# Kernel optimization log

Hardware: AMD Instinct MI355X
Metric: run time of the kernel (lower is better)

## Reference

```python
import jax, jax.numpy as jnp
import numpy as np
import itertools


def setup_inputs() -> dict:
    key = jax.random.key(0)
    k1, k2 = jax.random.split(key)
    vol = jax.random.normal(k1, (2, 160, 192, 224, 2), dtype=jnp.float32)
    trf = jax.random.normal(k2, (2, 160, 192, 224, 3), dtype=jnp.float32)
    return {"vol": vol, "trf": trf}


def _interpn_linear(vol, loc):
    """N-D multilinear interpolation of vol [*shape, C] at float locations.

    loc: list of ndims arrays, each [*shape], giving absolute sample coords.
    Out-of-domain points are clamped to the boundary (fill_value=None).
    Matches neurite's interpn('linear') math.
    """
    shape = vol.shape[:-1]
    ndims = len(shape)
    C = vol.shape[-1]
    maxs = [s - 1 for s in shape]

    # clip sample locations into the valid domain
    loc = [jnp.clip(l, 0.0, float(m)) for l, m in zip(loc, maxs)]
    loc0 = [jnp.clip(jnp.floor(l), 0.0, float(m)) for l, m in zip(loc, maxs)]
    loc1 = [jnp.clip(l0 + 1.0, 0.0, float(m)) for l0, m in zip(loc0, maxs)]
    # corner-0 weight is (loc1 - loc), corner-1 weight is its complement
    w_c0 = [l1 - l for l1, l in zip(loc1, loc)]
    w_c1 = [1.0 - w for w in w_c0]

    idx0 = [l.astype(jnp.int32) for l in loc0]
    idx1 = [l.astype(jnp.int32) for l in loc1]

    # row-major strides for flat gather
    strides = np.concatenate([np.cumprod(np.array(shape[::-1]))[::-1][1:], [1]]).astype(np.int32)
    vol_flat = vol.reshape(-1, C)

    out = jnp.zeros(shape + (C,), dtype=vol.dtype)
    for corner in itertools.product((0, 1), repeat=ndims):
        flat_idx = 0
        wt = 1.0
        for d in range(ndims):
            i = idx0[d] if corner[d] == 0 else idx1[d]
            w = w_c0[d] if corner[d] == 0 else w_c1[d]
            flat_idx = flat_idx + i * int(strides[d])
            wt = wt * w
        gathered = jnp.take(vol_flat, flat_idx, axis=0)  # [*shape, C]
        out = out + wt[..., None] * gathered
    return out


def reference(vol, trf):
    # single_transform=True: only the first batch element is used
    v = vol[0]   # [D1, D2, D3, C]
    t = trf[0]   # [D1, D2, D3, 3] dense shift (ij indexing)
    shape = v.shape[:-1]
    ndims = len(shape)
    # absolute sample locations = meshgrid + shift
    loc = []
    for d in range(ndims):
        ax = [1] * ndims
        ax[d] = shape[d]
        grid_d = jnp.arange(shape[d], dtype=t.dtype).reshape(ax)
        loc.append(grid_d + t[..., d])
    return _interpn_linear(v, loc)
```

## Files before the change

### kernel.cpp

```cpp
#include <hip/hip_runtime.h>


constexpr int D0 = 160, D1 = 192, D2 = 224;
constexpr int TI = 8, TJ = 8, TK = 16;
constexpr int GT_I = D0 / TI;
constexpr int GT_J = D1 / TJ;
constexpr int GT_K = D2 / TK;
constexpr int NBLOCKS = GT_I * GT_J * GT_K;
constexpr int CPX = NBLOCKS / 8;

typedef float float4u __attribute__((ext_vector_type(4), aligned(8)));
typedef float vfloat4 __attribute__((ext_vector_type(4)));

__device__ __forceinline__ float2 sample_one(const float2* __restrict__ vol2,
                                             float fi, float fj, float fk,
                                             float s0, float s1, float s2)
{
    float l0 = fminf(fmaxf(fi + s0, 0.0f), (float)(D0 - 1));
    float l1 = fminf(fmaxf(fj + s1, 0.0f), (float)(D1 - 1));
    float l2 = fminf(fmaxf(fk + s2, 0.0f), (float)(D2 - 1));

    float f0 = floorf(l0), f1 = floorf(l1), f2 = floorf(l2);
    float g0 = fminf(f0 + 1.0f, (float)(D0 - 1));
    float g1 = fminf(f1 + 1.0f, (float)(D1 - 1));
    float g2 = fminf(f2 + 1.0f, (float)(D2 - 1));

    float w0a = g0 - l0, w1a = g1 - l1, w2a = g2 - l2;
    float w0b = 1.0f - w0a, w1b = 1.0f - w1a, w2b = 1.0f - w2a;

    int i0 = (int)f0, j0 = (int)f1, k0 = (int)f2;
    int i1 = (int)g0, j1 = (int)g1;
    int kb = min(k0, D2 - 2);

    int r0 = i0 * (D1 * D2), r1 = i1 * (D1 * D2);
    int c0 = j0 * D2,        c1 = j1 * D2;

    float4u q00 = *(const float4u*)(vol2 + (r0 + c0 + kb));
    float4u q01 = *(const float4u*)(vol2 + (r0 + c1 + kb));
    float4u q10 = *(const float4u*)(vol2 + (r1 + c0 + kb));
    float4u q11 = *(const float4u*)(vol2 + (r1 + c1 + kb));

    float v00x = w2a * q00.x + w2b * q00.z, v00y = w2a * q00.y + w2b * q00.w;
    float v01x = w2a * q01.x + w2b * q01.z, v01y = w2a * q01.y + w2b * q01.w;
    float v10x = w2a * q10.x + w2b * q10.z, v10y = w2a * q10.y + w2b * q10.w;
    float v11x = w2a * q11.x + w2b * q11.z, v11y = w2a * q11.y + w2b * q11.w;

    float waa = w0a * w1a, wab = w0a * w1b, wba = w0b * w1a, wbb = w0b * w1b;
    float2 r;
    r.x = waa * v00x + wab * v01x + wba * v10x + wbb * v11x;
    r.y = waa * v00y + wab * v01y + wba * v10y + wbb * v11y;
    return r;
}

__global__ __launch_bounds__(256) void st_trilinear8_kernel(
    const float* __restrict__ vol,
    const float* __restrict__ trf,
    vfloat4* __restrict__ out)
{
    int b  = blockIdx.x;
    int sw = (b & 7) * CPX + (b >> 3);

    int tk = sw % GT_K;
    int tb = sw / GT_K;
    int tj = tb % GT_J;
    int ti = tb / GT_J;

    int tid = threadIdx.x;
    int kq  = tid & 3;
    int j_l = (tid >> 2) & 7;
    int i_l = tid >> 5;

    int i = ti * TI + i_l;
    int j = tj * TJ + j_l;
    int k = tk * TK + kq * 4;

    int v0 = (i * D1 + j) * D2 + k;
    int u  = v0 >> 1;

    const float* tp = trf + 3 * (size_t)v0;
    vfloat4 T0 = __builtin_nontemporal_load((const vfloat4*)tp);
    vfloat4 T1 = __builtin_nontemporal_load((const vfloat4*)(tp + 4));
    vfloat4 T2 = __builtin_nontemporal_load((const vfloat4*)(tp + 8));

    const float2* vol2 = (const float2*)vol;
    float fi = (float)i, fj = (float)j, fk = (float)k;

    float2 A = sample_one(vol2, fi, fj, fk,        T0.x, T0.y, T0.z);
    float2 B = sample_one(vol2, fi, fj, fk + 1.0f, T0.w, T1.x, T1.y);
    float2 C = sample_one(vol2, fi, fj, fk + 2.0f, T1.z, T1.w, T2.x);
    float2 D = sample_one(vol2, fi, fj, fk + 3.0f, T2.y, T2.z, T2.w);

    vfloat4 o0 = { A.x, A.y, B.x, B.y };
    vfloat4 o1 = { C.x, C.y, D.x, D.y };
    __builtin_nontemporal_store(o0, &out[u]);
    __builtin_nontemporal_store(o1, &out[u + 1]);
}

extern "C" void kernel_launch(void* const* d_in, const int* in_sizes, int n_in,
                              void* d_out, int out_size, void* d_ws, size_t ws_size,
                              hipStream_t stream) {
    const float* vol = (const float*)d_in[0];
    const float* trf = (const float*)d_in[1];
    vfloat4* out = (vfloat4*)d_out;

    st_trilinear8_kernel<<<NBLOCKS, 256, 0, stream>>>(vol, trf, out);
}
```

Baseline: 330.0 us.

## Stage volume tile with halo in LDS for trilinear gathers

Each block now loads a haloed tile of the volume into shared memory cooperatively, then samples from it when all corner indices fall inside the tile, falling back to global gathers otherwise. The block grows to 512 threads with a larger j tile. This aims to replace scattered global/L2 gathers with LDS reads, at the cost of extra redundant staging traffic, a block-wide barrier, and high LDS usage that limits occupancy.

```diff
diff --git a/kernel.cpp b/kernel.cpp
--- a/kernel.cpp
+++ b/kernel.cpp
@@ -2,17 +2,27 @@
 
 
 constexpr int D0 = 160, D1 = 192, D2 = 224;
-constexpr int TI = 8, TJ = 8, TK = 16;
+constexpr int TI = 8, TJ = 16, TK = 16;
 constexpr int GT_I = D0 / TI;
 constexpr int GT_J = D1 / TJ;
 constexpr int GT_K = D2 / TK;
 constexpr int NBLOCKS = GT_I * GT_J * GT_K;
 constexpr int CPX = NBLOCKS / 8;
 
+constexpr int HALO = 4;
+constexpr int RI = TI + 2 * HALO;
+constexpr int RJ = TJ + 2 * HALO;
+constexpr int RK = TK + 2 * HALO;
+constexpr int RKP = 25;
+constexpr int NTHREADS = 512;
+constexpr int STAGE_ITERS = (RI * RJ * (RK / 2)) / NTHREADS;
+
 typedef float float4u __attribute__((ext_vector_type(4), aligned(8)));
 typedef float vfloat4 __attribute__((ext_vector_type(4)));
 
 __device__ __forceinline__ float2 sample_one(const float2* __restrict__ vol2,
+                                             const float2* lds,
+                                             int bi, int bj, int bk,
                                              float fi, float fj, float fk,
                                              float s0, float s1, float s2)
 {
@@ -32,13 +42,33 @@
     int i1 = (int)g0, j1 = (int)g1;
     int kb = min(k0, D2 - 2);
 
-    int r0 = i0 * (D1 * D2), r1 = i1 * (D1 * D2);
-    int c0 = j0 * D2,        c1 = j1 * D2;
+    bool inr = (i0 >= bi) && (i1 <= bi + RI - 1) &&
+               (j0 >= bj) && (j1 <= bj + RJ - 1) &&
+               (kb >= bk) && (kb <= bk + RK - 2);
 
-    float4u q00 = *(const float4u*)(vol2 + (r0 + c0 + kb));
-    float4u q01 = *(const float4u*)(vol2 + (r0 + c1 + kb));
-    float4u q10 = *(const float4u*)(vol2 + (r1 + c0 + kb));
-    float4u q11 = *(const float4u*)(vol2 + (r1 + c1 + kb));
+    float4u q00, q01, q10, q11;
+    if (__builtin_expect(inr, 1)) {
+        int rk = kb - bk;
+        int a00 = ((i0 - bi) * RJ + (j0 - bj)) * RKP + rk;
+        int a01 = ((i0 - bi) * RJ + (j1 - bj)) * RKP + rk;
+        int a10 = ((i1 - bi) * RJ + (j0 - bj)) * RKP + rk;
+        int a11 = ((i1 - bi) * RJ + (j1 - bj)) * RKP + rk;
+        float2 p00a = lds[a00], p00b = lds[a00 + 1];
+        float2 p01a = lds[a01], p01b = lds[a01 + 1];
+        float2 p10a = lds[a10], p10b = lds[a10 + 1];
+        float2 p11a = lds[a11], p11b = lds[a11 + 1];
+        q00 = float4u{p00a.x, p00a.y, p00b.x, p00b.y};
+        q01 = float4u{p01a.x, p01a.y, p01b.x, p01b.y};
+        q10 = float4u{p10a.x, p10a.y, p10b.x, p10b.y};
+        q11 = float4u{p11a.x, p11a.y, p11b.x, p11b.y};
+    } else {
+        int r0 = i0 * (D1 * D2), r1 = i1 * (D1 * D2);
+        int c0 = j0 * D2,        c1 = j1 * D2;
+        q00 = *(const float4u*)(vol2 + (r0 + c0 + kb));
+        q01 = *(const float4u*)(vol2 + (r0 + c1 + kb));
+        q10 = *(const float4u*)(vol2 + (r1 + c0 + kb));
+        q11 = *(const float4u*)(vol2 + (r1 + c1 + kb));
+    }
 
     float v00x = w2a * q00.x + w2b * q00.z, v00y = w2a * q00.y + w2b * q00.w;
     float v01x = w2a * q01.x + w2b * q01.z, v01y = w2a * q01.y + w2b * q01.w;
@@ -52,28 +82,32 @@
     return r;
 }
 
-__global__ __launch_bounds__(256) void st_trilinear8_kernel(
+__global__ __launch_bounds__(NTHREADS) void st_lds_kernel(
     const float* __restrict__ vol,
     const float* __restrict__ trf,
     vfloat4* __restrict__ out)
 {
+    __shared__ float2 lds[RI * RJ * RKP];
+
     int b  = blockIdx.x;
     int sw = (b & 7) * CPX + (b >> 3);
-
     int tk = sw % GT_K;
     int tb = sw / GT_K;
     int tj = tb % GT_J;
     int ti = tb / GT_J;
 
+    int bi = min(max(ti * TI - HALO, 0), D0 - RI);
+    int bj = min(max(tj * TJ - HALO, 0), D1 - RJ);
+    int bk = min(max(tk * TK - HALO, 0), D2 - RK);
+
     int tid = threadIdx.x;
+
     int kq  = tid & 3;
-    int j_l = (tid >> 2) & 7;
-    int i_l = tid >> 5;
-
+    int j_l = (tid >> 2) & 15;
+    int i_l = tid >> 6;
     int i = ti * TI + i_l;
     int j = tj * TJ + j_l;
     int k = tk * TK + kq * 4;
-
     int v0 = (i * D1 + j) * D2 + k;
     int u  = v0 >> 1;
 
@@ -82,13 +116,30 @@
     vfloat4 T1 = __builtin_nontemporal_load((const vfloat4*)(tp + 4));
     vfloat4 T2 = __builtin_nontemporal_load((const vfloat4*)(tp + 8));
 
+    #pragma unroll
+    for (int n = 0; n < STAGE_ITERS; ++n) {
+        int f   = tid + NTHREADS * n;
+        int fir = f % 12;
+        int row = f / 12;
+        int rj  = row % RJ;
+        int ri  = row / RJ;
+        const float* src = vol +
+            ((size_t)((bi + ri) * D1 + (bj + rj)) * D2 + bk) * 2 + fir * 4;
+        float4u v = *(const float4u*)src;
+        int li = (ri * RJ + rj) * RKP + fir * 2;
+        lds[li]     = make_float2(v.x, v.y);
+        lds[li + 1] = make_float2(v.z, v.w);
+    }
+
+    __syncthreads();
+
     const float2* vol2 = (const float2*)vol;
     float fi = (float)i, fj = (float)j, fk = (float)k;
 
-    float2 A = sample_one(vol2, fi, fj, fk,        T0.x, T0.y, T0.z);
-    float2 B = sample_one(vol2, fi, fj, fk + 1.0f, T0.w, T1.x, T1.y);
-    float2 C = sample_one(vol2, fi, fj, fk + 2.0f, T1.z, T1.w, T2.x);
-    float2 D = sample_one(vol2, fi, fj, fk + 3.0f, T2.y, T2.z, T2.w);
+    float2 A = sample_one(vol2, lds, bi, bj, bk, fi, fj, fk,        T0.x, T0.y, T0.z);
+    float2 B = sample_one(vol2, lds, bi, bj, bk, fi, fj, fk + 1.0f, T0.w, T1.x, T1.y);
+    float2 C = sample_one(vol2, lds, bi, bj, bk, fi, fj, fk + 2.0f, T1.z, T1.w, T2.x);
+    float2 D = sample_one(vol2, lds, bi, bj, bk, fi, fj, fk + 3.0f, T2.y, T2.z, T2.w);
 
     vfloat4 o0 = { A.x, A.y, B.x, B.y };
     vfloat4 o1 = { C.x, C.y, D.x, D.y };
@@ -103,5 +154,5 @@
     const float* trf = (const float*)d_in[1];
     vfloat4* out = (vfloat4*)d_out;
 
-    st_trilinear8_kernel<<<NBLOCKS, 256, 0, stream>>>(vol, trf, out);
+    st_lds_kernel<<<NBLOCKS, NTHREADS, 0, stream>>>(vol, trf, out);
 }
```

Result: faster. 302.2 us (-8.4%).
